# Kernel tuning notes

Measured on AMD Instinct MI355X. Metric: run time of the kernel, lower is better.

## Reference

```python
import jax, jax.numpy as jnp
import numpy as np

N = 100000   # nodes
E = 100000   # hyperedges
M = 1600000  # incidences
IN_C = 128
HID = 128
OUT_C = 64
L = 2
EPS = 1e-5


def _layer_norm(x, g, b):
    m = jnp.mean(x, axis=-1, keepdims=True)
    v = jnp.mean((x - m) ** 2, axis=-1, keepdims=True)
    return (x - m) * jax.lax.rsqrt(v + EPS) * g + b


def setup_inputs() -> dict:
    key = jax.random.key(0)
    ks = jax.random.split(key, 16)
    s_in = 1.0 / np.sqrt(IN_C)
    s_h = 1.0 / np.sqrt(HID)
    return {
        "x": jax.random.normal(ks[0], (N, IN_C), jnp.float32),
        "x_e": jax.random.normal(ks[1], (E, IN_C), jnp.float32),
        "edge_index": jax.random.randint(ks[2], (2, M), 0, N, jnp.int32),
        "in_norm_g": jnp.ones((IN_C,), jnp.float32),
        "in_norm_b": jnp.zeros((IN_C,), jnp.float32),
        "in_proj_W": jax.random.normal(ks[3], (IN_C, HID), jnp.float32) * s_in,
        "in_proj_b": jnp.zeros((HID,), jnp.float32),
        "norm_g": jnp.ones((L, HID), jnp.float32),
        "norm_b": jnp.zeros((L, HID), jnp.float32),
        "conv_W": jax.random.normal(ks[4], (L, HID, HID), jnp.float32) * s_h,
        "conv_b": jnp.zeros((L, HID), jnp.float32),
        "lin_W": jax.random.normal(ks[5], (HID, OUT_C), jnp.float32) * s_h,
        "lin_b": jnp.zeros((OUT_C,), jnp.float32),
    }


def reference(x, x_e, edge_index, in_norm_g, in_norm_b, in_proj_W, in_proj_b,
              norm_g, norm_b, conv_W, conv_b, lin_W, lin_b):
    src, dst = edge_index[0], edge_index[1]  # node ids, hyperedge ids
    h = _layer_norm(x, in_norm_g, in_norm_b)
    h = jax.nn.leaky_relu(h @ in_proj_W + in_proj_b)  # dropout = identity (eval)

    # HypergraphConv degree normalizers (hyperedge_weight = 1)
    ones = jnp.ones((M,), h.dtype)
    degD = jax.ops.segment_sum(ones, src, num_segments=N)
    D = jnp.where(degD > 0, 1.0 / degD, 0.0)          # [N]
    degB = jax.ops.segment_sum(ones, dst, num_segments=E)
    B = jnp.where(degB > 0, 1.0 / degB, 0.0)          # [E]

    for i in range(L):
        hn = _layer_norm(h, norm_g[i], norm_b[i])
        xw = hn @ conv_W[i]                            # [N, HID]
        # node -> hyperedge: sum_j B[e] * xw[j]
        he = jax.ops.segment_sum(B[dst][:, None] * xw[src], dst, num_segments=E)
        # hyperedge -> node: sum_e D[n] * he[e]
        h2 = jax.ops.segment_sum(D[src][:, None] * he[dst], src, num_segments=N)
        h = jax.nn.leaky_relu(h2 + conv_b[i])

    # MinAggregation: segment-min of gathered node features per hyperedge
    agg = jax.ops.segment_min(h[src], dst, num_segments=E)  # [E, HID]
    return agg @ lin_W + lin_b                              # [E, OUT_C]
```

## Files before the change

kernel.cpp:

```cpp
#include <hip/hip_runtime.h>

#define NN 100000
#define NE 100000
#define MI 1600000
#define HID 128
#define OUTC 64
#define LSLOPE 0.01f
#define EPSV 1e-5f
#define ADJ_STRIDE 48

#define BUILD_PASSES 8
#define BUILD_WIN ((NN + BUILD_PASSES - 1) / BUILD_PASSES)
#define BUILD_ILP 8
#define BUILD_MB (256 * BUILD_ILP)
#define BUILD_NB ((MI + BUILD_MB - 1) / BUILD_MB)
#define WPREP_NB 224

typedef unsigned short us;
typedef __attribute__((ext_vector_type(4))) unsigned short us4;
typedef __attribute__((ext_vector_type(8))) unsigned short us8;
typedef __attribute__((ext_vector_type(8))) short short8;
typedef __attribute__((ext_vector_type(4))) float f32x4;
typedef __attribute__((ext_vector_type(16))) float f32x16;

__device__ __forceinline__ float bf2f(us h) {
    return __uint_as_float(((unsigned)h) << 16);
}
__device__ __forceinline__ us f2bf(float f) {
    unsigned u = __float_as_uint(f);
    return (us)((u + 0x7FFFu + ((u >> 16) & 1u)) >> 16);
}

__global__ __launch_bounds__(256) void build_all_kernel(
    const int* __restrict__ ei,
    int* __restrict__ cntE, int* __restrict__ cntN,
    int* __restrict__ adjE, int* __restrict__ adjN,
    const float* __restrict__ in_W, const float* __restrict__ conv_W,
    const float* __restrict__ lin_W,
    us* __restrict__ wt_in, us* __restrict__ wt_c0,
    us* __restrict__ wt_c1, us* __restrict__ wt_lin)
{
    const int t = threadIdx.x;
    if (blockIdx.x < WPREP_NB) {
        int idx = blockIdx.x * 256 + t;
        if (idx < 49152) {
            int mat = idx >> 14, r = idx & 16383;
            const float* src = mat == 0 ? in_W : (mat == 1 ? conv_W : conv_W + 16384);
            us* dst = mat == 0 ? wt_in : (mat == 1 ? wt_c0 : wt_c1);
            int n = r >> 7, k = r & 127;
            dst[r] = f2bf(src[k * 128 + n]);
        } else {
            int r = idx - 49152;
            int n = r >> 7, k = r & 127;
            float v = lin_W[k * 64 + n];
            us h = f2bf(v);
            wt_lin[r] = h;
            wt_lin[8192 + r] = f2bf(v - bf2f(h));
        }
        return;
    }
    const int local = blockIdx.x - WPREP_NB;
    const int pass = local & 7;
    const int mblk = local >> 3;
    const int lo = pass * BUILD_WIN;
    const int hi = lo + BUILD_WIN < NN ? lo + BUILD_WIN : NN;
    const int m0 = mblk * BUILD_MB + t * 8;
    if (m0 >= MI) return;
    int4 sa = *(const int4*)(ei + m0);
    int4 sb = *(const int4*)(ei + m0 + 4);
    int4 da = *(const int4*)(ei + MI + m0);
    int4 db = *(const int4*)(ei + MI + m0 + 4);
    int ss[8] = {sa.x, sa.y, sa.z, sa.w, sb.x, sb.y, sb.z, sb.w};
    int dd[8] = {da.x, da.y, da.z, da.w, db.x, db.y, db.z, db.w};
    #pragma unroll
    for (int k = 0; k < 8; ++k) {
        int s = ss[k], d = dd[k];
        if (d >= lo && d < hi) {
            int p = atomicAdd(&cntE[d], 1);
            if (p < ADJ_STRIDE) adjE[d * ADJ_STRIDE + p] = s;
        }
        if (s >= lo && s < hi) {
            int p = atomicAdd(&cntN[s], 1);
            if (p < ADJ_STRIDE) adjN[s * ADJ_STRIDE + p] = d;
        }
    }
}

template <int MODE>
__global__ __launch_bounds__(256) void gather_kernel(
    const int* __restrict__ cnt, const int* __restrict__ adj,
    const us* __restrict__ src, const float* __restrict__ bias,
    us* __restrict__ dst, int R)
{
    const int q = threadIdx.x >> 4;
    const int lane = threadIdx.x & 15;
    const int r = blockIdx.x * 16 + q;
    if (r >= R) return;
    const int nraw = cnt[r];
    int n = nraw < ADJ_STRIDE ? nraw : ADJ_STRIDE;
    const int* arow = adj + (size_t)r * ADJ_STRIDE;
    float a[8];
    #pragma unroll
    for (int k = 0; k < 8; ++k) a[k] = 0.f;
    const us* base = src + lane * 8;
    if (n > 0) {
        const int idx0 = arow[0];
        for (int j = 0; j < n; j += 16) {
            const int rem = n - j;
            int id[16];
            #pragma unroll
            for (int u4 = 0; u4 < 4; ++u4) {
                int4 i4 = *(const int4*)(arow + j + u4 * 4);
                id[u4 * 4 + 0] = i4.x; id[u4 * 4 + 1] = i4.y;
                id[u4 * 4 + 2] = i4.z; id[u4 * 4 + 3] = i4.w;
            }
            #pragma unroll
            for (int u = 0; u < 16; ++u) id[u] = u < rem ? id[u] : idx0;
            us8 v[16];
            #pragma unroll
            for (int u = 0; u < 16; ++u)
                v[u] = *(const us8*)(base + (size_t)id[u] * HID);
            #pragma unroll
            for (int u = 0; u < 16; ++u) {
                #pragma unroll
                for (int k = 0; k < 8; ++k) {
                    float f = bf2f(v[u][k]);
                    a[k] += (u < rem ? f : 0.f);
                }
            }
        }
    }
    float s = nraw > 0 ? 1.0f / (float)nraw : 0.f;
    if (MODE == 0) {
        #pragma unroll
        for (int k = 0; k < 8; ++k) a[k] *= s;
    } else {
        float4 b0 = *(const float4*)(bias + lane * 8);
        float4 b1 = *(const float4*)(bias + lane * 8 + 4);
        float bb[8] = {b0.x, b0.y, b0.z, b0.w, b1.x, b1.y, b1.z, b1.w};
        #pragma unroll
        for (int k = 0; k < 8; ++k) {
            float x = s * a[k] + bb[k];
            a[k] = x > 0.f ? x : LSLOPE * x;
        }
    }
    us8 o;
    #pragma unroll
    for (int k = 0; k < 8; ++k) o[k] = f2bf(a[k]);
    *(us8*)(dst + (size_t)r * HID + lane * 8) = o;
}

__global__ __launch_bounds__(256) void min_lin_kernel(
    const int* __restrict__ cnt, const int* __restrict__ adj,
    const us* __restrict__ src, const us* __restrict__ wt_lin,
    const float* __restrict__ lin_b, float* __restrict__ out)
{
    __shared__ us Amin[16 * 136];
    const int t = threadIdx.x;
    {
        const int q = t >> 4;
        const int lane = t & 15;
        const int r = blockIdx.x * 16 + q;
        const int nraw = cnt[r];
        int n = nraw < ADJ_STRIDE ? nraw : ADJ_STRIDE;
        const int* arow = adj + (size_t)r * ADJ_STRIDE;
        float a[8];
        #pragma unroll
        for (int k = 0; k < 8; ++k) a[k] = INFINITY;
        const us* base = src + lane * 8;
        if (n > 0) {
            const int idx0 = arow[0];
            for (int j = 0; j < n; j += 16) {
                const int rem = n - j;
                int id[16];
                #pragma unroll
                for (int u4 = 0; u4 < 4; ++u4) {
                    int4 i4 = *(const int4*)(arow + j + u4 * 4);
                    id[u4 * 4 + 0] = i4.x; id[u4 * 4 + 1] = i4.y;
                    id[u4 * 4 + 2] = i4.z; id[u4 * 4 + 3] = i4.w;
                }
                #pragma unroll
                for (int u = 0; u < 16; ++u) id[u] = u < rem ? id[u] : idx0;
                us8 v[16];
                #pragma unroll
                for (int u = 0; u < 16; ++u)
                    v[u] = *(const us8*)(base + (size_t)id[u] * HID);
                #pragma unroll
                for (int u = 0; u < 16; ++u) {
                    #pragma unroll
                    for (int k = 0; k < 8; ++k) {
                        float f = bf2f(v[u][k]);
                        a[k] = fminf(a[k], u < rem ? f : INFINITY);
                    }
                }
            }
        }
        us8 o;
        #pragma unroll
        for (int k = 0; k < 8; ++k) o[k] = f2bf(a[k]);
        *(us8*)(Amin + q * 136 + lane * 8) = o;
    }
    __syncthreads();
    const int l = t & 63;
    const int w = t >> 6;
    const int cr = l & 15;
    const int ko = (l >> 4) * 8;
    f32x4 acc = {0.f, 0.f, 0.f, 0.f};
    const us* Wb = wt_lin + (size_t)(w * 16 + cr) * 128 + ko;
    const us* Ab = Amin + cr * 136 + ko;
    #pragma unroll
    for (int ks = 0; ks < 4; ++ks) {
        short8 a  = *(const short8*)(Ab + ks * 32);
        short8 bh = *(const short8*)(Wb + ks * 32);
        short8 bl = *(const short8*)(Wb + 8192 + ks * 32);
        acc = __builtin_amdgcn_mfma_f32_16x16x32_bf16(a, bh, acc, 0, 0, 0);
        acc = __builtin_amdgcn_mfma_f32_16x16x32_bf16(a, bl, acc, 0, 0, 0);
    }
    const int gc = w * 16 + cr;
    const float bv = lin_b[gc];
    const int r0 = blockIdx.x * 16 + (l >> 4) * 4;
    #pragma unroll
    for (int j = 0; j < 4; ++j) {
        out[(size_t)(r0 + j) * OUTC + gc] = acc[j] + bv;
    }
}

template <int NC, bool ABF16, bool OBF16>
__global__ __launch_bounds__(512) void mfma_gemm_kernel(
    const void* __restrict__ Av, const float* __restrict__ ln_g, const float* __restrict__ ln_b,
    const us* __restrict__ WT, const float* __restrict__ bias,
    void* __restrict__ outv, int R, int flags)
{
    constexpr int SA = 136;
    constexpr int CT = NC / 64;
    __shared__ us As[128 * SA];
    __shared__ us Ws[NC * SA];
    __shared__ float red_s[512];
    __shared__ float red_q[512];
    __shared__ float r_mean[128];
    __shared__ float r_rstd[128];

    const int t = threadIdx.x;
    const int row0 = blockIdx.x * 128;

    constexpr int WUS4 = NC * 128 / 4;
    #pragma unroll
    for (int i = t; i < WUS4; i += 512) {
        us4 w = ((const us4*)WT)[i];
        int nrow = i >> 5, k4 = i & 31;
        *(us4*)(Ws + nrow * SA + k4 * 4) = w;
    }

    {
        const int r = t >> 2, sub = t & 3;
        const int gr = row0 + r;
        float v[32];
        if (gr < R) {
            if (ABF16) {
                const us* ap = (const us*)Av + (size_t)gr * 128 + sub * 32;
                #pragma unroll
                for (int j4 = 0; j4 < 8; ++j4) {
                    us4 x4 = *(const us4*)(ap + j4 * 4);
                    v[j4 * 4 + 0] = bf2f(x4.x); v[j4 * 4 + 1] = bf2f(x4.y);
                    v[j4 * 4 + 2] = bf2f(x4.z); v[j4 * 4 + 3] = bf2f(x4.w);
                }
            } else {
                const float* ap = (const float*)Av + (size_t)gr * 128 + sub * 32;
                #pragma unroll
                for (int j4 = 0; j4 < 8; ++j4) {
                    float4 f4 = *(const float4*)(ap + j4 * 4);
                    v[j4 * 4 + 0] = f4.x; v[j4 * 4 + 1] = f4.y;
                    v[j4 * 4 + 2] = f4.z; v[j4 * 4 + 3] = f4.w;
                }
            }
        } else {
            #pragma unroll
            for (int j = 0; j < 32; ++j) v[j] = 0.f;
        }
        if (flags & 1) {
            float s = 0.f, q = 0.f;
            #pragma unroll
            for (int j = 0; j < 32; ++j) { s += v[j]; q += v[j] * v[j]; }
            red_s[t] = s; red_q[t] = q;
            __syncthreads();
            if (t < 128) {
                float ss = red_s[t * 4] + red_s[t * 4 + 1] + red_s[t * 4 + 2] + red_s[t * 4 + 3];
                float qq = red_q[t * 4] + red_q[t * 4 + 1] + red_q[t * 4 + 2] + red_q[t * 4 + 3];
                float mu = ss * (1.0f / 128.0f);
                float var = qq * (1.0f / 128.0f) - mu * mu;
                r_mean[t] = mu;
                r_rstd[t] = rsqrtf(var + EPSV);
            }
            __syncthreads();
            float mu = r_mean[r], rs = r_rstd[r];
            #pragma unroll
            for (int j4 = 0; j4 < 8; ++j4) {
                float4 g4 = *(const float4*)(ln_g + sub * 32 + j4 * 4);
                float4 b4 = *(const float4*)(ln_b + sub * 32 + j4 * 4);
                v[j4 * 4 + 0] = (v[j4 * 4 + 0] - mu) * rs * g4.x + b4.x;
                v[j4 * 4 + 1] = (v[j4 * 4 + 1] - mu) * rs * g4.y + b4.y;
                v[j4 * 4 + 2] = (v[j4 * 4 + 2] - mu) * rs * g4.z + b4.z;
                v[j4 * 4 + 3] = (v[j4 * 4 + 3] - mu) * rs * g4.w + b4.w;
            }
        }
        #pragma unroll
        for (int j4 = 0; j4 < 8; ++j4) {
            us4 o;
            o.x = f2bf(v[j4 * 4 + 0]); o.y = f2bf(v[j4 * 4 + 1]);
            o.z = f2bf(v[j4 * 4 + 2]); o.w = f2bf(v[j4 * 4 + 3]);
            *(us4*)(As + r * SA + sub * 32 + j4 * 4) = o;
        }
    }
    __syncthreads();

    const int lane = t & 63;
    const int wave = t >> 6;
    const int wr = (wave & 3) * 32;
    const int wc = (wave >> 2) * (NC / 2);
    const int m = lane & 31;
    const int half = lane >> 5;
    const us* a_base = As + (wr + m) * SA + half * 8;

    f32x16 acc[CT];
    #pragma unroll
    for (int ct = 0; ct < CT; ++ct) acc[ct] = (f32x16)(0.0f);

    #pragma unroll
    for (int ks = 0; ks < 8; ++ks) {
        short8 a = *(const short8*)(a_base + ks * 16);
        #pragma unroll
        for (int ct = 0; ct < CT; ++ct) {
            const us* b_base = Ws + (wc + ct * 32 + m) * SA + half * 8 + ks * 16;
            short8 b = *(const short8*)b_base;
            acc[ct] = __builtin_amdgcn_mfma_f32_32x32x16_bf16(a, b, acc[ct], 0, 0, 0);
        }
    }

    #pragma unroll
    for (int ct = 0; ct < CT; ++ct) {
        int gc = wc + ct * 32 + m;
        float bv = bias ? bias[gc] : 0.f;
        #pragma unroll
        for (int reg = 0; reg < 16; ++reg) {
            int rloc = (reg & 3) + 8 * (reg >> 2) + 4 * half;
            int gr = row0 + wr + rloc;
            if (gr < R) {
                float y = acc[ct][reg] + bv;
                if (flags & 4) y = y > 0.f ? y : LSLOPE * y;
                if (OBF16) ((us*)outv)[(size_t)gr * NC + gc] = f2bf(y);
                else       ((float*)outv)[(size_t)gr * NC + gc] = y;
            }
        }
    }
}

extern "C" void kernel_launch(void* const* d_in, const int* in_sizes, int n_in,
                              void* d_out, int out_size, void* d_ws, size_t ws_size,
                              hipStream_t stream) {
    const float* x      = (const float*)d_in[0];
    const int*   ei     = (const int*)d_in[2];
    const float* in_g   = (const float*)d_in[3];
    const float* in_b   = (const float*)d_in[4];
    const float* in_W   = (const float*)d_in[5];
    const float* in_pb  = (const float*)d_in[6];
    const float* norm_g = (const float*)d_in[7];
    const float* norm_b = (const float*)d_in[8];
    const float* conv_W = (const float*)d_in[9];
    const float* conv_b = (const float*)d_in[10];
    const float* lin_W  = (const float*)d_in[11];
    const float* lin_b  = (const float*)d_in[12];
    float* out = (float*)d_out;

    us* h_bf   = (us*)d_ws;
    us* xw_bf  = h_bf  + (size_t)NN * HID;
    us* he_bf  = xw_bf + (size_t)NN * HID;
    int* cntE   = (int*)(he_bf + (size_t)NE * HID);
    int* cntN   = cntE + NE;
    int* adjE   = cntN + NN;
    int* adjN   = adjE + (size_t)NE * ADJ_STRIDE;
    us* wt_in  = (us*)(adjN + (size_t)NN * ADJ_STRIDE);
    us* wt_c0  = wt_in + 128 * 128;
    us* wt_c1  = wt_c0 + 128 * 128;
    us* wt_lin = wt_c1 + 128 * 128;

    hipMemsetAsync(cntE, 0, (size_t)(NN + NE) * sizeof(int), stream);
    build_all_kernel<<<WPREP_NB + BUILD_PASSES * BUILD_NB, 256, 0, stream>>>(
        ei, cntE, cntN, adjE, adjN, in_W, conv_W, lin_W, wt_in, wt_c0, wt_c1, wt_lin);

    mfma_gemm_kernel<HID, false, true><<<(NN + 127) / 128, 512, 0, stream>>>(
        x, in_g, in_b, wt_in, in_pb, h_bf, NN, 1 | 4);

    for (int i = 0; i < 2; ++i) {
        mfma_gemm_kernel<HID, true, true><<<(NN + 127) / 128, 512, 0, stream>>>(
            h_bf, norm_g + i * HID, norm_b + i * HID, i ? wt_c1 : wt_c0,
            nullptr, xw_bf, NN, 1);
        gather_kernel<0><<<(NE + 15) / 16, 256, 0, stream>>>(cntE, adjE, xw_bf, nullptr, he_bf, NE);
        gather_kernel<1><<<(NN + 15) / 16, 256, 0, stream>>>(cntN, adjN, he_bf, conv_b + i * HID, h_bf, NN);
    }

    min_lin_kernel<<<NE / 16, 256, 0, stream>>>(cntE, adjE, h_bf, wt_lin, lin_b, out);
}
```

Baseline: 709.2 us.

## Fuse layer-0 hyperedge-to-node gather with layer-1 LayerNorm and conv GEMM

Adds a kernel that gathers hyperedge features into node rows, applies bias and leaky ReLU, then LayerNorm and the layer-1 conv MFMA GEMM on a 128-row tile held in shared memory. This avoids writing h to global memory and reading it back in a separate GEMM launch. The gather loop is also moved into a shared device helper. The fused kernel uses about 70KB of LDS and 512 threads, which may lower occupancy for the latency-bound gather phase.

```diff
diff --git a/kernel.cpp b/kernel.cpp
--- a/kernel.cpp
+++ b/kernel.cpp
@@ -86,6 +86,41 @@
     }
 }
 
+template <bool MIN>
+__device__ __forceinline__ void gather_row(
+    const int* __restrict__ arow, int n, const us* __restrict__ base, float a[8])
+{
+    #pragma unroll
+    for (int k = 0; k < 8; ++k) a[k] = MIN ? INFINITY : 0.f;
+    if (n <= 0) return;
+    const int idx0 = arow[0];
+    for (int j = 0; j < n; j += 16) {
+        const int rem = n - j;
+        int id[16];
+        #pragma unroll
+        for (int u4 = 0; u4 < 4; ++u4) {
+            int4 i4 = *(const int4*)(arow + j + u4 * 4);
+            id[u4 * 4 + 0] = i4.x; id[u4 * 4 + 1] = i4.y;
+            id[u4 * 4 + 2] = i4.z; id[u4 * 4 + 3] = i4.w;
+        }
+        #pragma unroll
+        for (int u = 0; u < 16; ++u) id[u] = u < rem ? id[u] : idx0;
+        us8 v[16];
+        #pragma unroll
+        for (int u = 0; u < 16; ++u)
+            v[u] = *(const us8*)(base + (size_t)id[u] * HID);
+        #pragma unroll
+        for (int u = 0; u < 16; ++u) {
+            #pragma unroll
+            for (int k = 0; k < 8; ++k) {
+                float f = bf2f(v[u][k]);
+                if (MIN) a[k] = fminf(a[k], u < rem ? f : INFINITY);
+                else     a[k] += (u < rem ? f : 0.f);
+            }
+        }
+    }
+}
+
 template <int MODE>
 __global__ __launch_bounds__(256) void gather_kernel(
     const int* __restrict__ cnt, const int* __restrict__ adj,
@@ -98,38 +133,8 @@
     if (r >= R) return;
     const int nraw = cnt[r];
     int n = nraw < ADJ_STRIDE ? nraw : ADJ_STRIDE;
-    const int* arow = adj + (size_t)r * ADJ_STRIDE;
     float a[8];
-    #pragma unroll
-    for (int k = 0; k < 8; ++k) a[k] = 0.f;
-    const us* base = src + lane * 8;
-    if (n > 0) {
-        const int idx0 = arow[0];
-        for (int j = 0; j < n; j += 16) {
-            const int rem = n - j;
-            int id[16];
-            #pragma unroll
-            for (int u4 = 0; u4 < 4; ++u4) {
-                int4 i4 = *(const int4*)(arow + j + u4 * 4);
-                id[u4 * 4 + 0] = i4.x; id[u4 * 4 + 1] = i4.y;
-                id[u4 * 4 + 2] = i4.z; id[u4 * 4 + 3] = i4.w;
-            }
-            #pragma unroll
-            for (int u = 0; u < 16; ++u) id[u] = u < rem ? id[u] : idx0;
-            us8 v[16];
-            #pragma unroll
-            for (int u = 0; u < 16; ++u)
-                v[u] = *(const us8*)(base + (size_t)id[u] * HID);
-            #pragma unroll
-            for (int u = 0; u < 16; ++u) {
-                #pragma unroll
-                for (int k = 0; k < 8; ++k) {
-                    float f = bf2f(v[u][k]);
-                    a[k] += (u < rem ? f : 0.f);
-                }
-            }
-        }
-    }
+    gather_row<false>(adj + (size_t)r * ADJ_STRIDE, n, src + lane * 8, a);
     float s = nraw > 0 ? 1.0f / (float)nraw : 0.f;
     if (MODE == 0) {
         #pragma unroll
@@ -148,6 +153,140 @@
     #pragma unroll
     for (int k = 0; k < 8; ++k) o[k] = f2bf(a[k]);
     *(us8*)(dst + (size_t)r * HID + lane * 8) = o;
+}
+
+__global__ __launch_bounds__(512) void gather_ln_gemm_kernel(
+    const int* __restrict__ cnt, const int* __restrict__ adj,
+    const us* __restrict__ src, const float* __restrict__ gbias,
+    const float* __restrict__ ln_g, const float* __restrict__ ln_b,
+    const us* __restrict__ WT, us* __restrict__ outv, int R)
+{
+    constexpr int SA = 136;
+    __shared__ us As[128 * SA];
+    __shared__ us Ws[128 * SA];
+    __shared__ float red_s[512];
+    __shared__ float red_q[512];
+    __shared__ float r_mean[128];
+    __shared__ float r_rstd[128];
+
+    const int t = threadIdx.x;
+    const int row0 = blockIdx.x * 128;
+
+    #pragma unroll
+    for (int i = t; i < 128 * 128 / 4; i += 512) {
+        us4 w = ((const us4*)WT)[i];
+        int nrow = i >> 5, k4 = i & 31;
+        *(us4*)(Ws + nrow * SA + k4 * 4) = w;
+    }
+
+    {
+        const int lane = t & 15;
+        const int rq = t >> 4;
+        const float* gb = gbias + lane * 8;
+        for (int it = 0; it < 4; ++it) {
+            const int rl = it * 32 + rq;
+            const int r = row0 + rl;
+            float a[8];
+            int nraw = 0;
+            if (r < R) {
+                nraw = cnt[r];
+                int n = nraw < ADJ_STRIDE ? nraw : ADJ_STRIDE;
+                gather_row<false>(adj + (size_t)r * ADJ_STRIDE, n, src + lane * 8, a);
+            } else {
+                #pragma unroll
+                for (int k = 0; k < 8; ++k) a[k] = 0.f;
+            }
+            const float s = nraw > 0 ? 1.0f / (float)nraw : 0.f;
+            us8 o;
+            #pragma unroll
+            for (int k = 0; k < 8; ++k) {
+                float x = s * a[k] + gb[k];
+                x = x > 0.f ? x : LSLOPE * x;
+                o[k] = f2bf(x);
+            }
+            *(us8*)(As + rl * SA + lane * 8) = o;
+        }
+    }
+    __syncthreads();
+
+    {
+        const int r = t >> 2, sub = t & 3;
+        float v[32];
+        {
+            const us* ap = As + r * SA + sub * 32;
+            #pragma unroll
+            for (int j4 = 0; j4 < 8; ++j4) {
+                us4 x4 = *(const us4*)(ap + j4 * 4);
+                v[j4 * 4 + 0] = bf2f(x4.x); v[j4 * 4 + 1] = bf2f(x4.y);
+                v[j4 * 4 + 2] = bf2f(x4.z); v[j4 * 4 + 3] = bf2f(x4.w);
+            }
+        }
+        float s = 0.f, q = 0.f;
+        #pragma unroll
+        for (int j = 0; j < 32; ++j) { s += v[j]; q += v[j] * v[j]; }
+        red_s[t] = s; red_q[t] = q;
+        __syncthreads();
+        if (t < 128) {
+            float ss = red_s[t * 4] + red_s[t * 4 + 1] + red_s[t * 4 + 2] + red_s[t * 4 + 3];
+            float qq = red_q[t * 4] + red_q[t * 4 + 1] + red_q[t * 4 + 2] + red_q[t * 4 + 3];
+            float mu = ss * (1.0f / 128.0f);
+            float var = qq * (1.0f / 128.0f) - mu * mu;
+            r_mean[t] = mu;
+            r_rstd[t] = rsqrtf(var + EPSV);
+        }
+        __syncthreads();
+        float mu = r_mean[r], rs = r_rstd[r];
+        #pragma unroll
+        for (int j4 = 0; j4 < 8; ++j4) {
+            float4 g4 = *(const float4*)(ln_g + sub * 32 + j4 * 4);
+            float4 b4 = *(const float4*)(ln_b + sub * 32 + j4 * 4);
+            v[j4 * 4 + 0] = (v[j4 * 4 + 0] - mu) * rs * g4.x + b4.x;
+            v[j4 * 4 + 1] = (v[j4 * 4 + 1] - mu) * rs * g4.y + b4.y;
+            v[j4 * 4 + 2] = (v[j4 * 4 + 2] - mu) * rs * g4.z + b4.z;
+            v[j4 * 4 + 3] = (v[j4 * 4 + 3] - mu) * rs * g4.w + b4.w;
+        }
+        #pragma unroll
+        for (int j4 = 0; j4 < 8; ++j4) {
+            us4 o;
+            o.x = f2bf(v[j4 * 4 + 0]); o.y = f2bf(v[j4 * 4 + 1]);
+            o.z = f2bf(v[j4 * 4 + 2]); o.w = f2bf(v[j4 * 4 + 3]);
+            *(us4*)(As + r * SA + sub * 32 + j4 * 4) = o;
+        }
+    }
+    __syncthreads();
+
+    const int l = t & 63;
+    const int wave = t >> 6;
+    const int wr = (wave & 3) * 32;
+    const int wc = (wave >> 2) * 64;
+    const int m = l & 31;
+    const int half = l >> 5;
+    const us* a_base = As + (wr + m) * SA + half * 8;
+
+    f32x16 acc[2];
+    #pragma unroll
+    for (int ct = 0; ct < 2; ++ct) acc[ct] = (f32x16)(0.0f);
+
+    #pragma unroll
+    for (int ks = 0; ks < 8; ++ks) {
+        short8 a = *(const short8*)(a_base + ks * 16);
+        #pragma unroll
+        for (int ct = 0; ct < 2; ++ct) {
+            const us* b_base = Ws + (wc + ct * 32 + m) * SA + half * 8 + ks * 16;
+            short8 b = *(const short8*)b_base;
+            acc[ct] = __builtin_amdgcn_mfma_f32_32x32x16_bf16(a, b, acc[ct], 0, 0, 0);
+        }
+    }
+    #pragma unroll
+    for (int ct = 0; ct < 2; ++ct) {
+        int gc = wc + ct * 32 + m;
+        #pragma unroll
+        for (int reg = 0; reg < 16; ++reg) {
+            int rloc = (reg & 3) + 8 * (reg >> 2) + 4 * half;
+            int gr = row0 + wr + rloc;
+            if (gr < R) outv[(size_t)gr * HID + gc] = f2bf(acc[ct][reg]);
+        }
+    }
 }
 
 __global__ __launch_bounds__(256) void min_lin_kernel(
@@ -163,38 +302,8 @@
         const int r = blockIdx.x * 16 + q;
         const int nraw = cnt[r];
         int n = nraw < ADJ_STRIDE ? nraw : ADJ_STRIDE;
-        const int* arow = adj + (size_t)r * ADJ_STRIDE;
         float a[8];
-        #pragma unroll
-        for (int k = 0; k < 8; ++k) a[k] = INFINITY;
-        const us* base = src + lane * 8;
-        if (n > 0) {
-            const int idx0 = arow[0];
-            for (int j = 0; j < n; j += 16) {
-                const int rem = n - j;
-                int id[16];
-                #pragma unroll
-                for (int u4 = 0; u4 < 4; ++u4) {
-                    int4 i4 = *(const int4*)(arow + j + u4 * 4);
-                    id[u4 * 4 + 0] = i4.x; id[u4 * 4 + 1] = i4.y;
-                    id[u4 * 4 + 2] = i4.z; id[u4 * 4 + 3] = i4.w;
-                }
-                #pragma unroll
-                for (int u = 0; u < 16; ++u) id[u] = u < rem ? id[u] : idx0;
-                us8 v[16];
-                #pragma unroll
-                for (int u = 0; u < 16; ++u)
-                    v[u] = *(const us8*)(base + (size_t)id[u] * HID);
-                #pragma unroll
-                for (int u = 0; u < 16; ++u) {
-                    #pragma unroll
-                    for (int k = 0; k < 8; ++k) {
-                        float f = bf2f(v[u][k]);
-                        a[k] = fminf(a[k], u < rem ? f : INFINITY);
-                    }
-                }
-            }
-        }
+        gather_row<true>(adj + (size_t)r * ADJ_STRIDE, n, src + lane * 8, a);
         us8 o;
         #pragma unroll
         for (int k = 0; k < 8; ++k) o[k] = f2bf(a[k]);
@@ -390,13 +499,15 @@
     mfma_gemm_kernel<HID, false, true><<<(NN + 127) / 128, 512, 0, stream>>>(
         x, in_g, in_b, wt_in, in_pb, h_bf, NN, 1 | 4);
 
-    for (int i = 0; i < 2; ++i) {
-        mfma_gemm_kernel<HID, true, true><<<(NN + 127) / 128, 512, 0, stream>>>(
-            h_bf, norm_g + i * HID, norm_b + i * HID, i ? wt_c1 : wt_c0,
-            nullptr, xw_bf, NN, 1);
-        gather_kernel<0><<<(NE + 15) / 16, 256, 0, stream>>>(cntE, adjE, xw_bf, nullptr, he_bf, NE);
-        gather_kernel<1><<<(NN + 15) / 16, 256, 0, stream>>>(cntN, adjN, he_bf, conv_b + i * HID, h_bf, NN);
-    }
+    mfma_gemm_kernel<HID, true, true><<<(NN + 127) / 128, 512, 0, stream>>>(
+        h_bf, norm_g, norm_b, wt_c0, nullptr, xw_bf, NN, 1);
+    gather_kernel<0><<<(NE + 15) / 16, 256, 0, stream>>>(cntE, adjE, xw_bf, nullptr, he_bf, NE);
+
+    gather_ln_gemm_kernel<<<(NN + 127) / 128, 512, 0, stream>>>(
+        cntN, adjN, he_bf, conv_b, norm_g + HID, norm_b + HID, wt_c1, xw_bf, NN);
+
+    gather_kernel<0><<<(NE + 15) / 16, 256, 0, stream>>>(cntE, adjE, xw_bf, nullptr, he_bf, NE);
+    gather_kernel<1><<<(NN + 15) / 16, 256, 0, stream>>>(cntN, adjN, he_bf, conv_b + HID, h_bf, NN);
 
     min_lin_kernel<<<NE / 16, 256, 0, stream>>>(cntE, adjE, h_bf, wt_lin, lin_b, out);
 }
```

Measured after the change: 703.7 us. About the same (-0.8%).
